# Performance work log

Hardware: AMD Instinct MI355X
Metric: run time of the kernel (lower is better)

## Reference

```python
import jax, jax.numpy as jnp
import numpy as np

B, IN_DIM, L = 8, 1, 512
D_MODEL, N_LAYERS, D_STATE, HORIZON, D_CONV, EXPAND = 512, 4, 16, 96, 4, 2
D_INNER = EXPAND * D_MODEL            # 1024
DT_RANK = (D_MODEL + 15) // 16        # ceil(d_model/16) = 32
EPS = 1e-5


def setup_inputs() -> dict:
    key = jax.random.key(0)
    ks = jax.random.split(key, 10)
    s = 0.02
    f32 = jnp.float32
    return {
        "x": jax.random.normal(ks[0], (B, IN_DIM, L), f32),
        "embed_w": jax.random.normal(ks[1], (D_MODEL, IN_DIM), f32) * s,
        "embed_b": jnp.zeros((D_MODEL,), f32),
        "norm_w": jnp.ones((N_LAYERS, D_MODEL), f32),
        "in_proj_w": jax.random.normal(ks[2], (N_LAYERS, 2 * D_INNER, D_MODEL), f32) * s,
        "conv_w": jax.random.normal(ks[3], (N_LAYERS, D_INNER, D_CONV), f32) * s,
        "conv_b": jnp.zeros((N_LAYERS, D_INNER), f32),
        "x_proj_w": jax.random.normal(ks[4], (N_LAYERS, DT_RANK + 2 * D_STATE, D_INNER), f32) * s,
        "dt_w": jax.random.normal(ks[5], (N_LAYERS, D_INNER, DT_RANK), f32) * s,
        "dt_b": jax.random.uniform(ks[6], (N_LAYERS, D_INNER), f32, -4.0, -2.0),
        "A_log": jnp.log(jnp.broadcast_to(jnp.arange(1, D_STATE + 1, dtype=f32), (N_LAYERS, D_INNER, D_STATE))),
        "D": jnp.ones((N_LAYERS, D_INNER), f32),
        "out_proj_w": jax.random.normal(ks[7], (N_LAYERS, D_MODEL, D_INNER), f32) * s,
        "head_w": jax.random.normal(ks[8], (HORIZON, D_MODEL), f32) * s,
        "head_b": jnp.zeros((HORIZON,), f32),
    }


def _rmsnorm(x, w):
    return x * jax.lax.rsqrt(jnp.mean(x * x, axis=-1, keepdims=True) + EPS) * w


def _mamba_layer(x, norm_w, in_w, conv_w, conv_b, xproj_w, dt_w, dt_b, A_log, Dp, out_w):
    res = x
    h = _rmsnorm(x, norm_w)
    xz = h @ in_w.T                       # (B, L, 2*I)
    xin, z = jnp.split(xz, 2, axis=-1)
    # causal depthwise conv1d over L (left-pad d_conv-1)
    lhs = jnp.swapaxes(xin, 1, 2)         # (B, I, L)
    rhs = conv_w[:, None, :]              # (I, 1, K)
    conv = jax.lax.conv_general_dilated(
        lhs, rhs, (1,), [(D_CONV - 1, 0)],
        dimension_numbers=("NCH", "OIH", "NCH"), feature_group_count=D_INNER)
    xin = jax.nn.silu(jnp.swapaxes(conv, 1, 2) + conv_b)   # (B, L, I)
    dbc = xin @ xproj_w.T                                   # (B, L, dt_rank+2N)
    delta = jax.nn.softplus(dbc[..., :DT_RANK] @ dt_w.T + dt_b)  # (B, L, I)
    Bc = dbc[..., DT_RANK:DT_RANK + D_STATE]                # (B, L, N)
    Cc = dbc[..., DT_RANK + D_STATE:]                       # (B, L, N)
    A = -jnp.exp(A_log)                                     # (I, N)
    dA = jnp.exp(delta[..., None] * A)                      # (B, L, I, N)
    dBx = delta[..., None] * Bc[:, :, None, :] * xin[..., None]

    def step(hst, inputs):
        a, bx = inputs
        hst = a * hst + bx
        return hst, hst

    h0 = jnp.zeros((x.shape[0], D_INNER, D_STATE), x.dtype)
    _, hs = jax.lax.scan(step, h0, (jnp.swapaxes(dA, 0, 1), jnp.swapaxes(dBx, 0, 1)))
    hs = jnp.swapaxes(hs, 0, 1)                             # (B, L, I, N)
    y = jnp.einsum("blin,bln->bli", hs, Cc) + Dp * xin
    y = y * jax.nn.silu(z)
    return res + y @ out_w.T


def reference(x, embed_w, embed_b, norm_w, in_proj_w, conv_w, conv_b, x_proj_w,
              dt_w, dt_b, A_log, D, out_proj_w, head_w, head_b):
    h = jnp.swapaxes(x, 1, 2) @ embed_w.T + embed_b         # (B, L, d_model)
    for i in range(N_LAYERS):
        h = _mamba_layer(h, norm_w[i], in_proj_w[i], conv_w[i], conv_b[i],
                         x_proj_w[i], dt_w[i], dt_b[i], A_log[i], D[i], out_proj_w[i])
    return h[:, -1, :] @ head_w.T + head_b                  # (B, horizon)
```

## Files before the change

kernel.cpp:

```cpp
#include <hip/hip_runtime.h>
#include <hip/hip_bf16.h>

#define B_  8
#define L_  512
#define DM  512
#define NL  4
#define DS  16
#define HOR 96
#define DC  4
#define DI  1024
#define DTR 32

#define CHUNK 16
#define NCHK (L_/CHUNK)

typedef __bf16 bf16_t;
typedef __bf16 b8_t __attribute__((ext_vector_type(8)));
typedef __bf16 b4_t __attribute__((ext_vector_type(4)));
typedef float  f4_t __attribute__((ext_vector_type(4)));

#define LOG2E 1.44269504088896f

__device__ __forceinline__ float sigmoidf_(float x){ return 1.f/(1.f+__expf(-x)); }

__device__ __forceinline__ void async16(const bf16_t* g, bf16_t* l){
  __builtin_amdgcn_global_load_lds((const __attribute__((address_space(1))) void*)g,
                                   (__attribute__((address_space(3))) void*)l, 16, 0, 0);
}

__global__ __launch_bounds__(256) void k_prep(const float* __restrict__ p0, bf16_t* __restrict__ o0,
                                              const float* __restrict__ p1, bf16_t* __restrict__ o1,
                                              const float* __restrict__ p2, bf16_t* __restrict__ o2,
                                              const float* __restrict__ p3, bf16_t* __restrict__ o3,
                                              const float* __restrict__ x, const float* __restrict__ ew,
                                              const float* __restrict__ eb, float* __restrict__ h,
                                              const float* __restrict__ nw, bf16_t* __restrict__ hbf,
                                              float* __restrict__ sumsq){
  int blk = blockIdx.x;
  if (blk < 6528){
    int j = blk*256 + threadIdx.x;
    const int S0=1048576, S1=65536, S2=32768;
    const float* src; bf16_t* dst;
    const float* fold = nullptr;
    if (j < S0){
      src=p0; dst=o0;
      int idx4 = j<<2;
      fold = nw + ((idx4>>20)*DM) + (idx4 & (DM-1));
    }
    else if ((j-=S0) < S1){ src=p1; dst=o1; }
    else if ((j-=S1) < S2){ src=p2; dst=o2; }
    else { j-=S2; src=p3; dst=o3; }
    f4_t v = ((const f4_t*)src)[j];
    if (fold){ f4_t f = *(const f4_t*)fold; v *= f; }
    bf16_t* o = dst + (size_t)j*4;
    o[0]=(bf16_t)v[0]; o[1]=(bf16_t)v[1]; o[2]=(bf16_t)v[2]; o[3]=(bf16_t)v[3];
  } else {
    int tid = threadIdx.x;
    int j = (blk-6528)*256 + tid;
    int idx = j*4;
    int d = idx & (DM-1); int t = idx >> 9;
    float xv = x[t];
    f4_t w = *(const f4_t*)(ew + d);
    f4_t b = *(const f4_t*)(eb + d);
    f4_t v;
    #pragma unroll
    for (int c=0;c<4;c++) v[c] = xv*w[c] + b[c];
    *(f4_t*)(h + idx) = v;
    b4_t hv;
    #pragma unroll
    for (int c=0;c<4;c++) hv[c] = (bf16_t)v[c];
    *(b4_t*)(hbf + idx) = hv;
    float s = v[0]*v[0]+v[1]*v[1]+v[2]*v[2]+v[3]*v[3];
    #pragma unroll
    for (int m=32;m;m>>=1) s += __shfl_xor(s, m);
    __shared__ float red2[4];
    if ((tid&63)==0) red2[tid>>6] = s;
    __syncthreads();
    int tb = (blk-6528)*2;
    if (tid==0)   sumsq[tb]   = red2[0]+red2[1];
    if (tid==128) sumsq[tb+1] = red2[2]+red2[3];
  }
}

__global__ __launch_bounds__(256) void k_g128(const bf16_t* __restrict__ A, int lda,
                                              const bf16_t* __restrict__ W, int ldw,
                                              bf16_t* __restrict__ Cbf, int ldc,
                                              const float* __restrict__ sumsq){
  __shared__ __align__(16) bf16_t As[2][2*4096];
  __shared__ __align__(16) bf16_t Ws[2][2*4096];
  int tid = threadIdx.x;
  int m0 = blockIdx.y*128, n0 = blockIdx.x*128;
  int wave = tid>>6, lane = tid&63;
  int wm = (wave>>1)*64, wn = (wave&1)*64;
  int lr = lane&15, q = lane>>4;
  int srow = tid>>2;
  int scol = (tid&3)*8;
  f4_t acc[4][4] = {};
  auto stage = [&](int buf, int k0){
    #pragma unroll
    for (int s=0;s<4;s++){
      int hh = s>>1, p = s&1;
      int row = hh*64 + srow;
      async16(A + (size_t)(m0+row)*lda + k0 + p*32 + scol,
              &As[buf][p*4096 + row*32 + scol]);
      async16(W + (size_t)(n0+row)*ldw + k0 + p*32 + scol,
              &Ws[buf][p*4096 + row*32 + scol]);
    }
  };
  stage(0, 0);
  #pragma unroll
  for (int it=0; it<8; ++it){
    if (it<7){
      stage((it+1)&1, (it+1)*64);
      asm volatile("s_waitcnt vmcnt(8)" ::: "memory");
    } else {
      asm volatile("s_waitcnt vmcnt(0)" ::: "memory");
    }
    __builtin_amdgcn_s_barrier();
    int buf = it&1;
    __builtin_amdgcn_s_setprio(1);
    #pragma unroll
    for (int p=0;p<2;p++){
      b8_t a[4], b[4];
      #pragma unroll
      for (int i=0;i<4;i++) a[i] = *(const b8_t*)(&As[buf][p*4096 + (wm+i*16+lr)*32 + q*8]);
      #pragma unroll
      for (int j=0;j<4;j++) b[j] = *(const b8_t*)(&Ws[buf][p*4096 + (wn+j*16+lr)*32 + q*8]);
      #pragma unroll
      for (int i=0;i<4;i++)
        #pragma unroll
        for (int j=0;j<4;j++)
          acc[i][j] = __builtin_amdgcn_mfma_f32_16x16x32_bf16(a[i], b[j], acc[i][j], 0,0,0);
    }
    __builtin_amdgcn_s_setprio(0);
    __builtin_amdgcn_s_barrier();
  }
  #pragma unroll
  for (int i=0;i<4;i++){
    int rb = m0 + wm + i*16 + q*4;
    f4_t sc;
    #pragma unroll
    for (int r=0;r<4;r++) sc[r] = rsqrtf(sumsq[rb+r]*(1.f/DM) + 1e-5f);
    #pragma unroll
    for (int j=0;j<4;j++){
      int col = n0 + wn + j*16 + lr;
      #pragma unroll
      for (int r=0;r<4;r++)
        Cbf[(size_t)(rb+r)*ldc + col] = (bf16_t)(acc[i][j][r]*sc[r]);
    }
  }
}

__global__ __launch_bounds__(256) void k_gout(const bf16_t* __restrict__ A,
                                              const bf16_t* __restrict__ W,
                                              float* __restrict__ C,
                                              bf16_t* __restrict__ hbf,
                                              float* __restrict__ sumsq){
  __shared__ __align__(16) char sm[65536];
  bf16_t* As = (bf16_t*)sm;
  bf16_t* Ws = (bf16_t*)(sm + 32768);
  float*  red = (float*)sm;
  int tid = threadIdx.x;
  int m0 = blockIdx.y*64, n0 = blockIdx.x*64;
  int wave = tid>>6, lane = tid&63;
  int lr = lane&15, q = lane>>4;
  f4_t acc[4][4] = {};
  auto stage = [&](int buf, int k0){
    #pragma unroll
    for (int p=0;p<4;p++){
      async16(A + (size_t)(m0+(tid>>2))*DI + k0 + p*32 + (tid&3)*8,
              As + buf*8192 + p*2048 + tid*8);
      async16(W + (size_t)(n0+(tid>>2))*DI + k0 + p*32 + (tid&3)*8,
              Ws + buf*8192 + p*2048 + tid*8);
    }
  };
  stage(0, 0);
  #pragma unroll
  for (int it=0; it<8; ++it){
    if (it<7){
      stage((it+1)&1, (it+1)*128);
      asm volatile("s_waitcnt vmcnt(8)" ::: "memory");
    } else {
      asm volatile("s_waitcnt vmcnt(0)" ::: "memory");
    }
    __builtin_amdgcn_s_barrier();
    int buf = it&1;
    const bf16_t* Ap = As + buf*8192 + wave*2048;
    const bf16_t* Wp = Ws + buf*8192 + wave*2048;
    b8_t a[4], b[4];
    #pragma unroll
    for (int i=0;i<4;i++) a[i] = *(const b8_t*)(Ap + (i*16+lr)*32 + q*8);
    #pragma unroll
    for (int j=0;j<4;j++) b[j] = *(const b8_t*)(Wp + (j*16+lr)*32 + q*8);
    __builtin_amdgcn_s_setprio(1);
    #pragma unroll
    for (int i=0;i<4;i++)
      #pragma unroll
      for (int j=0;j<4;j++)
        acc[i][j] = __builtin_amdgcn_mfma_f32_16x16x32_bf16(a[i], b[j], acc[i][j], 0,0,0);
    __builtin_amdgcn_s_setprio(0);
    __builtin_amdgcn_s_barrier();
  }
  #pragma unroll
  for (int i=0;i<4;i++)
  #pragma unroll
  for (int j=0;j<4;j++)
  #pragma unroll
  for (int r=0;r<4;r++){
    int rl = i*16 + q*4 + r;
    int t4 = ((rl ^ (rl>>2)) & 3) << 2;
    int c4 = j*4 + (lr>>2);
    red[wave*4096 + rl*64 + ((c4 ^ t4)<<2) + (lr&3)] = acc[i][j][r];
  }
  __syncthreads();
  #pragma unroll
  for (int g=0;g<4;g++){
    int row = g*16 + (tid>>4);
    int t4 = ((row ^ (row>>2)) & 3) << 2;
    int fo = row*64 + (((tid&15) ^ t4) << 2);
    f4_t v = *(const f4_t*)(red + fo);
    v += *(const f4_t*)(red + 4096 + fo);
    v += *(const f4_t*)(red + 8192 + fo);
    v += *(const f4_t*)(red + 12288 + fo);
    size_t off = (size_t)(m0+row)*DM + n0 + (tid&15)*4;
    f4_t c = *(const f4_t*)(C + off);
    c += v;
    *(f4_t*)(C + off) = c;
    b4_t hv;
    #pragma unroll
    for (int k=0;k<4;k++) hv[k] = (bf16_t)c[k];
    *(b4_t*)(hbf + off) = hv;
    float s2 = c[0]*c[0]+c[1]*c[1]+c[2]*c[2]+c[3]*c[3];
    s2 += __shfl_xor(s2,1); s2 += __shfl_xor(s2,2);
    s2 += __shfl_xor(s2,4); s2 += __shfl_xor(s2,8);
    if ((tid&15)==0) atomicAdd(sumsq + m0 + row, s2);
  }
}

__global__ __launch_bounds__(256) void k_dbc(const bf16_t* __restrict__ xzbf, const float* __restrict__ cw,
                                             const float* __restrict__ cb, const bf16_t* __restrict__ wxp,
                                             float* __restrict__ part, bf16_t* __restrict__ xinbf){
  __shared__ bf16_t As[4*64*32];
  __shared__ bf16_t Ws[4*64*32];
  int tid = threadIdx.x;
  int m0 = blockIdx.x*64;
  int z = blockIdx.y;
  int kbase = z*128;
  int wave = tid>>6, lane = tid&63;
  int wm = (wave>>1)*32, wn = (wave&1)*32;
  int lr = lane&15, q = lane>>4;
  int e0 = tid*8, r0 = e0>>5, c0 = e0&31;
  int gt = m0 + r0;
  int l  = gt & (L_-1);
  f4_t acc[2][2] = {};
  #pragma unroll
  for (int p=0;p<4;p++){
    int ch = kbase + p*32 + c0;
    float cv[8];
    #pragma unroll
    for (int c=0;c<8;c++) cv[c] = cb[ch+c];
    #pragma unroll
    for (int k=0;k<DC;k++){
      if (l + k - (DC-1) >= 0){
        b8_t xv = *(const b8_t*)(xzbf + (size_t)(gt + k - (DC-1))*(2*DI) + ch);
        #pragma unroll
        for (int c=0;c<8;c++) cv[c] += (float)xv[c] * cw[(ch+c)*DC + k];
      }
    }
    b8_t av;
    #pragma unroll
    for (int c=0;c<8;c++){ float s = cv[c]*sigmoidf_(cv[c]); av[c] = (bf16_t)s; }
    *(b8_t*)(As + p*2048 + e0) = av;
    *(b8_t*)(xinbf + (size_t)gt*DI + ch) = av;
    async16(wxp + (size_t)r0*DI + kbase + p*32 + c0, Ws + p*2048 + e0);
  }
  __syncthreads();
  #pragma unroll
  for (int p=0;p<4;p++){
    b8_t a[2], b[2];
    #pragma unroll
    for (int i=0;i<2;i++) a[i] = *(const b8_t*)(As + p*2048 + (wm+i*16+lr)*32 + q*8);
    #pragma unroll
    for (int j=0;j<2;j++) b[j] = *(const b8_t*)(Ws + p*2048 + (wn+j*16+lr)*32 + q*8);
    #pragma unroll
    for (int i=0;i<2;i++)
      #pragma unroll
      for (int j=0;j<2;j++)
        acc[i][j] = __builtin_amdgcn_mfma_f32_16x16x32_bf16(a[i], b[j], acc[i][j], 0,0,0);
  }
  float* P = part + (size_t)z*(B_*L_*64);
  #pragma unroll
  for (int i=0;i<2;i++)
  #pragma unroll
  for (int j=0;j<2;j++){
    int col = wn + j*16 + lr;
    int rb  = m0 + wm + i*16 + q*4;
    #pragma unroll
    for (int r=0;r<4;r++) P[(size_t)(rb+r)*64 + col] = acc[i][j][r];
  }
}

__global__ __launch_bounds__(256) void k_dt(const float* __restrict__ part, const bf16_t* __restrict__ wdt,
                                            const float* __restrict__ dtb, float* __restrict__ dbc,
                                            bf16_t* __restrict__ delta){
  __shared__ bf16_t As[64*32];
  __shared__ bf16_t Ws[64*32];
  int tid = threadIdx.x;
  int m0 = blockIdx.y*64, n0 = blockIdx.x*64;
  const size_t S = (size_t)B_*L_*64;
  int r0 = tid>>2, c0 = (tid&3)*8;
  int gt = m0 + r0;
  size_t base = (size_t)gt*64 + c0;
  f4_t s0 = *(const f4_t*)(part + base);
  f4_t s1 = *(const f4_t*)(part + base + 4);
  #pragma unroll
  for (int z=1;z<8;z++){
    s0 += *(const f4_t*)(part + z*S + base);
    s1 += *(const f4_t*)(part + z*S + base + 4);
  }
  b8_t av;
  #pragma unroll
  for (int c=0;c<4;c++){ av[c] = (bf16_t)s0[c]; av[4+c] = (bf16_t)s1[c]; }
  *(b8_t*)(As + tid*8) = av;
  if (n0 == 0){
    f4_t t0 = *(const f4_t*)(part + base + 32);
    f4_t t1 = *(const f4_t*)(part + base + 36);
    #pragma unroll
    for (int z=1;z<8;z++){
      t0 += *(const f4_t*)(part + z*S + base + 32);
      t1 += *(const f4_t*)(part + z*S + base + 36);
    }
    *(f4_t*)(dbc + base + 32) = t0;
    *(f4_t*)(dbc + base + 36) = t1;
  }
  async16(wdt + (size_t)(n0+r0)*DTR + c0, Ws + tid*8);
  __syncthreads();
  int wave = tid>>6, lane = tid&63;
  int wm = (wave>>1)*32, wn = (wave&1)*32;
  int lr = lane&15, q = lane>>4;
  b8_t a[2], b[2];
  #pragma unroll
  for (int i=0;i<2;i++) a[i] = *(const b8_t*)(As + (wm+i*16+lr)*32 + q*8);
  #pragma unroll
  for (int j=0;j<2;j++) b[j] = *(const b8_t*)(Ws + (wn+j*16+lr)*32 + q*8);
  f4_t acc[2][2] = {};
  #pragma unroll
  for (int i=0;i<2;i++)
    #pragma unroll
    for (int j=0;j<2;j++)
      acc[i][j] = __builtin_amdgcn_mfma_f32_16x16x32_bf16(a[i], b[j], acc[i][j], 0,0,0);
  #pragma unroll
  for (int i=0;i<2;i++)
  #pragma unroll
  for (int j=0;j<2;j++){
    int col = n0 + wn + j*16 + lr;
    int rb  = m0 + wm + i*16 + q*4;
    #pragma unroll
    for (int r=0;r<4;r++){
      float xv = acc[i][j][r] + dtb[col];
      float v = (xv>20.f)?xv:log1pf(__expf(xv));
      delta[(size_t)(rb+r)*DI + col] = (bf16_t)v;
    }
  }
}

__global__ __launch_bounds__(256) void k_scan_p1(const bf16_t* __restrict__ delta, const bf16_t* __restrict__ xin,
                                                 const float* __restrict__ dbc, const float* __restrict__ Alog,
                                                 bf16_t* __restrict__ hend, bf16_t* __restrict__ aprod){
  __shared__ bf16_t des[CHUNK][256];
  __shared__ bf16_t xs[CHUNK][256];
  __shared__ float Bs[CHUNK][DS];
  int tid = threadIdx.x;
  int blk = blockIdx.x;
  int chgrp = blk & 3;
  int chunk = (blk>>2) & (NCHK-1);
  int b = blk >> 7;
  int ch0 = chgrp<<8;
  int ch = ch0 + tid;
  int t0 = (b<<9) + chunk*CHUNK;
  #pragma unroll
  for (int idx=tid; idx<CHUNK*32; idx+=256){
    int row = idx>>5, c = (idx&31)*8;
    *(b8_t*)(&des[row][c]) = *(const b8_t*)(delta + (size_t)(t0+row)*DI + ch0 + c);
    *(b8_t*)(&xs[row][c])  = *(const b8_t*)(xin   + (size_t)(t0+row)*DI + ch0 + c);
  }
  {
    int ll = tid>>4, n = tid&15;
    Bs[ll][n] = dbc[(t0+ll)*64 + DTR + n];
  }
  __syncthreads();
  float An2[DS], h[DS];
  const f4_t* Ap = (const f4_t*)(Alog + ch*DS);
  #pragma unroll
  for (int v=0;v<4;v++){
    f4_t a4 = Ap[v];
    #pragma unroll
    for (int k=0;k<4;k++){ An2[v*4+k] = -__expf(a4[k])*LOG2E; h[v*4+k]=0.f; }
  }
  float sde = 0.f;
  #pragma unroll
  for (int l=0;l<CHUNK;l++){
    float de = (float)des[l][tid];
    float xv = (float)xs[l][tid];
    float dx = de*xv;
    sde += de;
    #pragma unroll
    for (int n=0;n<DS;n++){
      float dA = exp2f(de*An2[n]);
      h[n] = dA*h[n] + dx*Bs[l][n];
    }
  }
  size_t base = ((size_t)chunk*(B_*DI) + (b<<10) + ch)*DS;
  b8_t hv[2], av[2];
  #pragma unroll
  for (int v=0;v<2;v++)
    #pragma unroll
    for (int k=0;k<8;k++){
      hv[v][k] = (bf16_t)h[v*8+k];
      av[v][k] = (bf16_t)exp2f(An2[v*8+k]*sde);
    }
  ((b8_t*)(hend + base))[0] = hv[0]; ((b8_t*)(hend + base))[1] = hv[1];
  ((b8_t*)(aprod + base))[0] = av[0]; ((b8_t*)(aprod + base))[1] = av[1];
}

__global__ __launch_bounds__(256) void k_scan_p2(const bf16_t* __restrict__ hend, bf16_t* __restrict__ ap_hin,
                                                 float* __restrict__ sumsq){
  if (blockIdx.x < 16) sumsq[(blockIdx.x<<8) | threadIdx.x] = 0.f;
  int g = blockIdx.x*256 + threadIdx.x;
  float h = 0.f;
  for (int c=0;c<NCHK;c++){
    size_t off = (size_t)c*(B_*DI*DS) + g;
    float a = (float)ap_hin[off];
    float e = (float)hend[off];
    ap_hin[off] = (bf16_t)h;
    h = a*h + e;
  }
}

__global__ __launch_bounds__(256) void k_scan_p3(const bf16_t* __restrict__ delta, const bf16_t* __restrict__ xz,
                                                 const bf16_t* __restrict__ xin,
                                                 const float* __restrict__ dbc, const float* __restrict__ Alog,
                                                 const bf16_t* __restrict__ hin, const float* __restrict__ Dp,
                                                 bf16_t* __restrict__ ybf){
  __shared__ bf16_t des[CHUNK][256];
  __shared__ bf16_t xs[CHUNK][256];
  __shared__ bf16_t zs[CHUNK][256];
  __shared__ float Bs[CHUNK][DS];
  __shared__ float Cs[CHUNK][DS];
  int tid = threadIdx.x;
  int blk = blockIdx.x;
  int chgrp = blk & 3;
  int chunk = (blk>>2) & (NCHK-1);
  int b = blk >> 7;
  int ch0 = chgrp<<8;
  int ch = ch0 + tid;
  int t0 = (b<<9) + chunk*CHUNK;
  #pragma unroll
  for (int idx=tid; idx<CHUNK*32; idx+=256){
    int row = idx>>5, c = (idx&31)*8;
    *(b8_t*)(&des[row][c]) = *(const b8_t*)(delta + (size_t)(t0+row)*DI + ch0 + c);
    *(b8_t*)(&xs[row][c])  = *(const b8_t*)(xin   + (size_t)(t0+row)*DI + ch0 + c);
    *(b8_t*)(&zs[row][c])  = *(const b8_t*)(xz + (size_t)(t0+row)*(2*DI) + DI + ch0 + c);
  }
  {
    int ll = tid>>4, n = tid&15;
    Bs[ll][n] = dbc[(t0+ll)*64 + DTR + n];
    Cs[ll][n] = dbc[(t0+ll)*64 + DTR + DS + n];
  }
  __syncthreads();
  float An2[DS], h[DS];
  const f4_t* Ap = (const f4_t*)(Alog + ch*DS);
  size_t base = ((size_t)chunk*(B_*DI) + (b<<10) + ch)*DS;
  b8_t h0 = ((const b8_t*)(hin + base))[0];
  b8_t h1 = ((const b8_t*)(hin + base))[1];
  #pragma unroll
  for (int v=0;v<4;v++){
    f4_t a4 = Ap[v];
    #pragma unroll
    for (int k=0;k<4;k++){
      An2[v*4+k] = -__expf(a4[k])*LOG2E;
      int idx = v*4+k;
      h[idx] = (idx<8) ? (float)h0[idx] : (float)h1[idx-8];
    }
  }
  float Dv = Dp[ch];
  bf16_t* yp = ybf + (size_t)t0*DI + ch;
  #pragma unroll
  for (int l=0;l<CHUNK;l++){
    float de = (float)des[l][tid];
    float zv = (float)zs[l][tid];
    float xv = (float)xs[l][tid];
    float dx = de*xv;
    float y = 0.f;
    #pragma unroll
    for (int n=0;n<DS;n++){
      float dA = exp2f(de*An2[n]);
      h[n] = dA*h[n] + dx*Bs[l][n];
      y += h[n]*Cs[l][n];
    }
    y = (y + Dv*xv) * (zv * sigmoidf_(zv));
    yp[(size_t)l*DI] = (bf16_t)y;
  }
}

__global__ __launch_bounds__(256) void k_head(const float* __restrict__ h, const float* __restrict__ hw,
                                              const float* __restrict__ hb, float* __restrict__ out){
  int wave = threadIdx.x>>6, lane = threadIdx.x&63;
  int gw = blockIdx.x*4 + wave;
  int b = gw / HOR, hh = gw % HOR;
  const float* hp = h + ((size_t)b*L_ + (L_-1))*DM;
  const float* wp = hw + (size_t)hh*DM;
  float s = 0.f;
  #pragma unroll
  for (int k=0;k<DM;k+=64) s += hp[k+lane]*wp[k+lane];
  #pragma unroll
  for (int m=32;m;m>>=1) s += __shfl_xor(s, m);
  if (lane==0) out[gw] = s + hb[hh];
}

extern "C" void kernel_launch(void* const* d_in, const int* in_sizes, int n_in,
                              void* d_out, int out_size, void* d_ws, size_t ws_size,
                              hipStream_t stream){
  const float* x    = (const float*)d_in[0];
  const float* ew   = (const float*)d_in[1];
  const float* eb   = (const float*)d_in[2];
  const float* nw   = (const float*)d_in[3];
  const float* ipw  = (const float*)d_in[4];
  const float* cw   = (const float*)d_in[5];
  const float* cb   = (const float*)d_in[6];
  const float* xpw  = (const float*)d_in[7];
  const float* dtw  = (const float*)d_in[8];
  const float* dtb  = (const float*)d_in[9];
  const float* alog = (const float*)d_in[10];
  const float* Dp   = (const float*)d_in[11];
  const float* opw  = (const float*)d_in[12];
  const float* hw   = (const float*)d_in[13];
  const float* hb   = (const float*)d_in[14];
  float* out = (float*)d_out;

  char* ws = (char*)d_ws;
  size_t o = 0;
  float*  h      = (float*)(ws + o);  o += (size_t)8<<20;
  bf16_t* hbf    = (bf16_t*)(ws + o); o += (size_t)4<<20;
  bf16_t* xzbf   = (bf16_t*)(ws + o); o += (size_t)16<<20;
  bf16_t* xinbf  = (bf16_t*)(ws + o); o += (size_t)8<<20;
  bf16_t* delta  = (bf16_t*)(ws + o); o += (size_t)8<<20;
  bf16_t* ybf    = (bf16_t*)(ws + o); o += (size_t)8<<20;
  float*  dbc    = (float*)(ws + o);  o += (size_t)1<<20;
  float*  dbcp   = (float*)(ws + o);  o += (size_t)8<<20;
  bf16_t* w_in   = (bf16_t*)(ws + o); o += (size_t)8<<20;
  bf16_t* w_out  = (bf16_t*)(ws + o); o += (size_t)4<<20;
  bf16_t* w_xp   = (bf16_t*)(ws + o); o += (size_t)1<<19;
  bf16_t* w_dt   = (bf16_t*)(ws + o); o += (size_t)1<<18;
  bf16_t* hend   = (bf16_t*)(ws + o); o += (size_t)8<<20;
  bf16_t* aphin  = (bf16_t*)(ws + o); o += (size_t)8<<20;
  float*  sumsq  = (float*)(ws + o);  o += (size_t)1<<16;

  k_prep<<<8576,256,0,stream>>>(ipw, w_in, xpw, w_xp, dtw, w_dt, opw, w_out,
                                x, ew, eb, h, nw, hbf, sumsq);

  for (int i=0;i<NL;i++){
    k_g128<<<dim3(2*DI/128, B_*L_/128),256,0,stream>>>(
        hbf, DM, w_in + (size_t)i*2*DI*DM, DM, xzbf, 2*DI, sumsq);
    k_dbc<<<dim3(B_*L_/64, 8),256,0,stream>>>(xzbf, cw + i*DI*DC, cb + i*DI,
                                              w_xp + (size_t)i*64*DI, dbcp, xinbf);
    k_dt<<<dim3(DI/64, B_*L_/64),256,0,stream>>>(dbcp, w_dt + (size_t)i*DI*DTR,
                                                 dtb + i*DI, dbc, delta);
    k_scan_p1<<<B_*NCHK*4,256,0,stream>>>(delta, xinbf, dbc, alog + i*DI*DS, hend, aphin);
    k_scan_p2<<<(B_*DI*DS)/256,256,0,stream>>>(hend, aphin, sumsq);
    k_scan_p3<<<B_*NCHK*4,256,0,stream>>>(delta, xzbf, xinbf, dbc, alog + i*DI*DS,
                                          aphin, Dp + i*DI, ybf);
    k_gout<<<dim3(DM/64, B_*L_/64),256,0,stream>>>(ybf, w_out + (size_t)i*DM*DI, h, hbf, sumsq);
  }
  k_head<<<(B_*HOR)/4,256,0,stream>>>(h, hw, hb, out);
}
```

Measured before the change: 599.4 us.

## Split dt partial reduction into its own kernel, swizzle GEMM blocks, vectorize scan pass 2

Before, every column block of k_dt re-summed the eight split-K x_proj partials for its rows, so the same partial sums were read many times over. A new k_red kernel now does that reduction once, writing a bf16 dt input and the fp32 B/C values, and k_dt becomes a wider 64x256 MFMA tile that reads the compact bf16 buffer. The in_proj and out_proj GEMMs now use a 1D grid remapped so that neighbouring tiles land on the same XCD, which is meant to improve L2 reuse. k_scan_p2 handles four states per thread with vector loads, which cuts launched threads by four and may lower latency hiding in this sequential loop.

```diff
diff --git a/kernel.cpp b/kernel.cpp
--- a/kernel.cpp
+++ b/kernel.cpp
@@ -89,7 +89,10 @@
   __shared__ __align__(16) bf16_t As[2][2*4096];
   __shared__ __align__(16) bf16_t Ws[2][2*4096];
   int tid = threadIdx.x;
-  int m0 = blockIdx.y*128, n0 = blockIdx.x*128;
+  int bid = blockIdx.x;
+  int xcd = bid & 7, cch = bid >> 3;
+  int m0 = ((xcd<<2) + (cch>>4))*128;
+  int n0 = (cch & 15)*128;
   int wave = tid>>6, lane = tid&63;
   int wm = (wave>>1)*64, wn = (wave&1)*64;
   int lr = lane&15, q = lane>>4;
@@ -161,7 +164,10 @@
   bf16_t* Ws = (bf16_t*)(sm + 32768);
   float*  red = (float*)sm;
   int tid = threadIdx.x;
-  int m0 = blockIdx.y*64, n0 = blockIdx.x*64;
+  int bid = blockIdx.x;
+  int xcd = bid & 7, cch = bid >> 3;
+  int m0 = ((xcd<<3) + (cch>>3))*64;
+  int n0 = (cch & 7)*64;
   int wave = tid>>6, lane = tid&63;
   int lr = lane&15, q = lane>>4;
   f4_t acc[4][4] = {};
@@ -300,61 +306,60 @@
   }
 }
 
-__global__ __launch_bounds__(256) void k_dt(const float* __restrict__ part, const bf16_t* __restrict__ wdt,
-                                            const float* __restrict__ dtb, float* __restrict__ dbc,
+__global__ __launch_bounds__(256) void k_red(const float* __restrict__ part,
+                                             bf16_t* __restrict__ dbc_a,
+                                             float* __restrict__ dbc){
+  const size_t S = (size_t)B_*L_*64;
+  int idx = blockIdx.x*256 + threadIdx.x;
+  int token = idx>>4, c4 = idx&15;
+  size_t base = (size_t)token*64 + c4*4;
+  f4_t s = *(const f4_t*)(part + base);
+  #pragma unroll
+  for (int z=1;z<8;z++) s += *(const f4_t*)(part + z*S + base);
+  if (c4 < 8){
+    b4_t v;
+    #pragma unroll
+    for (int c=0;c<4;c++) v[c] = (bf16_t)s[c];
+    *(b4_t*)(dbc_a + (size_t)token*DTR + c4*4) = v;
+  } else {
+    *(f4_t*)(dbc + base) = s;
+  }
+}
+
+__global__ __launch_bounds__(256) void k_dt(const bf16_t* __restrict__ dbc_a,
+                                            const bf16_t* __restrict__ wdt,
+                                            const float* __restrict__ dtb,
                                             bf16_t* __restrict__ delta){
-  __shared__ bf16_t As[64*32];
-  __shared__ bf16_t Ws[64*32];
+  __shared__ __align__(16) bf16_t As[64*32];
+  __shared__ __align__(16) bf16_t Ws[256*32];
   int tid = threadIdx.x;
-  int m0 = blockIdx.y*64, n0 = blockIdx.x*64;
-  const size_t S = (size_t)B_*L_*64;
-  int r0 = tid>>2, c0 = (tid&3)*8;
-  int gt = m0 + r0;
-  size_t base = (size_t)gt*64 + c0;
-  f4_t s0 = *(const f4_t*)(part + base);
-  f4_t s1 = *(const f4_t*)(part + base + 4);
-  #pragma unroll
-  for (int z=1;z<8;z++){
-    s0 += *(const f4_t*)(part + z*S + base);
-    s1 += *(const f4_t*)(part + z*S + base + 4);
-  }
-  b8_t av;
-  #pragma unroll
-  for (int c=0;c<4;c++){ av[c] = (bf16_t)s0[c]; av[4+c] = (bf16_t)s1[c]; }
-  *(b8_t*)(As + tid*8) = av;
-  if (n0 == 0){
-    f4_t t0 = *(const f4_t*)(part + base + 32);
-    f4_t t1 = *(const f4_t*)(part + base + 36);
-    #pragma unroll
-    for (int z=1;z<8;z++){
-      t0 += *(const f4_t*)(part + z*S + base + 32);
-      t1 += *(const f4_t*)(part + z*S + base + 36);
-    }
-    *(f4_t*)(dbc + base + 32) = t0;
-    *(f4_t*)(dbc + base + 36) = t1;
-  }
-  async16(wdt + (size_t)(n0+r0)*DTR + c0, Ws + tid*8);
+  int m0 = blockIdx.y*64, n0 = blockIdx.x*256;
+  async16(dbc_a + (size_t)(m0 + (tid>>2))*DTR + (tid&3)*8, As + tid*8);
+  #pragma unroll
+  for (int s=0;s<4;s++){
+    int row = s*64 + (tid>>2);
+    async16(wdt + (size_t)(n0+row)*DTR + (tid&3)*8, Ws + row*32 + (tid&3)*8);
+  }
   __syncthreads();
   int wave = tid>>6, lane = tid&63;
-  int wm = (wave>>1)*32, wn = (wave&1)*32;
   int lr = lane&15, q = lane>>4;
-  b8_t a[2], b[2];
-  #pragma unroll
-  for (int i=0;i<2;i++) a[i] = *(const b8_t*)(As + (wm+i*16+lr)*32 + q*8);
-  #pragma unroll
-  for (int j=0;j<2;j++) b[j] = *(const b8_t*)(Ws + (wn+j*16+lr)*32 + q*8);
-  f4_t acc[2][2] = {};
-  #pragma unroll
-  for (int i=0;i<2;i++)
-    #pragma unroll
-    for (int j=0;j<2;j++)
+  b8_t a[4], b[4];
+  #pragma unroll
+  for (int i=0;i<4;i++) a[i] = *(const b8_t*)(As + (i*16+lr)*32 + q*8);
+  #pragma unroll
+  for (int j=0;j<4;j++) b[j] = *(const b8_t*)(Ws + (wave*64 + j*16+lr)*32 + q*8);
+  f4_t acc[4][4] = {};
+  #pragma unroll
+  for (int i=0;i<4;i++)
+    #pragma unroll
+    for (int j=0;j<4;j++)
       acc[i][j] = __builtin_amdgcn_mfma_f32_16x16x32_bf16(a[i], b[j], acc[i][j], 0,0,0);
   #pragma unroll
-  for (int i=0;i<2;i++)
-  #pragma unroll
-  for (int j=0;j<2;j++){
-    int col = n0 + wn + j*16 + lr;
-    int rb  = m0 + wm + i*16 + q*4;
+  for (int i=0;i<4;i++)
+  #pragma unroll
+  for (int j=0;j<4;j++){
+    int col = n0 + wave*64 + j*16 + lr;
+    int rb  = m0 + i*16 + q*4;
     #pragma unroll
     for (int r=0;r<4;r++){
       float xv = acc[i][j][r] + dtb[col];
@@ -426,14 +431,19 @@
 __global__ __launch_bounds__(256) void k_scan_p2(const bf16_t* __restrict__ hend, bf16_t* __restrict__ ap_hin,
                                                  float* __restrict__ sumsq){
   if (blockIdx.x < 16) sumsq[(blockIdx.x<<8) | threadIdx.x] = 0.f;
-  int g = blockIdx.x*256 + threadIdx.x;
-  float h = 0.f;
+  int g4 = blockIdx.x*256 + threadIdx.x;
+  size_t base = (size_t)g4*4;
+  float h[4] = {0.f,0.f,0.f,0.f};
   for (int c=0;c<NCHK;c++){
-    size_t off = (size_t)c*(B_*DI*DS) + g;
-    float a = (float)ap_hin[off];
-    float e = (float)hend[off];
-    ap_hin[off] = (bf16_t)h;
-    h = a*h + e;
+    size_t off = (size_t)c*(B_*DI*DS) + base;
+    b4_t a = *(const b4_t*)(ap_hin + off);
+    b4_t e = *(const b4_t*)(hend + off);
+    b4_t w;
+    #pragma unroll
+    for (int k=0;k<4;k++) w[k] = (bf16_t)h[k];
+    *(b4_t*)(ap_hin + off) = w;
+    #pragma unroll
+    for (int k=0;k<4;k++) h[k] = (float)a[k]*h[k] + (float)e[k];
   }
 }
 
@@ -555,22 +565,24 @@
   bf16_t* hend   = (bf16_t*)(ws + o); o += (size_t)8<<20;
   bf16_t* aphin  = (bf16_t*)(ws + o); o += (size_t)8<<20;
   float*  sumsq  = (float*)(ws + o);  o += (size_t)1<<16;
+  bf16_t* dbc_a  = (bf16_t*)(ws + o); o += (size_t)1<<18;
 
   k_prep<<<8576,256,0,stream>>>(ipw, w_in, xpw, w_xp, dtw, w_dt, opw, w_out,
                                 x, ew, eb, h, nw, hbf, sumsq);
 
   for (int i=0;i<NL;i++){
-    k_g128<<<dim3(2*DI/128, B_*L_/128),256,0,stream>>>(
+    k_g128<<<512,256,0,stream>>>(
         hbf, DM, w_in + (size_t)i*2*DI*DM, DM, xzbf, 2*DI, sumsq);
     k_dbc<<<dim3(B_*L_/64, 8),256,0,stream>>>(xzbf, cw + i*DI*DC, cb + i*DI,
                                               w_xp + (size_t)i*64*DI, dbcp, xinbf);
-    k_dt<<<dim3(DI/64, B_*L_/64),256,0,stream>>>(dbcp, w_dt + (size_t)i*DI*DTR,
-                                                 dtb + i*DI, dbc, delta);
+    k_red<<<256,256,0,stream>>>(dbcp, dbc_a, dbc);
+    k_dt<<<dim3(4, B_*L_/64),256,0,stream>>>(dbc_a, w_dt + (size_t)i*DI*DTR,
+                                             dtb + i*DI, delta);
     k_scan_p1<<<B_*NCHK*4,256,0,stream>>>(delta, xinbf, dbc, alog + i*DI*DS, hend, aphin);
-    k_scan_p2<<<(B_*DI*DS)/256,256,0,stream>>>(hend, aphin, sumsq);
+    k_scan_p2<<<128,256,0,stream>>>(hend, aphin, sumsq);
     k_scan_p3<<<B_*NCHK*4,256,0,stream>>>(delta, xzbf, xinbf, dbc, alog + i*DI*DS,
                                           aphin, Dp + i*DI, ybf);
-    k_gout<<<dim3(DM/64, B_*L_/64),256,0,stream>>>(ybf, w_out + (size_t)i*DM*DI, h, hbf, sumsq);
+    k_gout<<<512,256,0,stream>>>(ybf, w_out + (size_t)i*DM*DI, h, hbf, sumsq);
   }
   k_head<<<(B_*HOR)/4,256,0,stream>>>(h, hw, hb, out);
 }
```

Result: slower. 613.8 us (+2.4%).
